# Kernel tuning notes

Measured on AMD Instinct MI355X. Metric: run time of the kernel, lower is better.

Reference implementation:

```python
import jax, jax.numpy as jnp
import numpy as np

NUM_HEADS = 12

def setup_inputs() -> dict:
    key = jax.random.key(0)
    ks = jax.random.split(key, 8)
    B, N, C = 8, 1024, 768
    s = 1.0 / np.sqrt(C)
    return {
        "x": jax.random.normal(ks[0], (B, N, C), jnp.float32),
        "head_mask": jnp.ones((B, NUM_HEADS), jnp.float32),
        "q_w": jax.random.normal(ks[1], (C, C), jnp.float32) * s,
        "q_b": jnp.zeros((C,), jnp.float32),
        "k_w": jax.random.normal(ks[2], (C, C), jnp.float32) * s,
        "k_b": jnp.zeros((C,), jnp.float32),
        "v_w": jax.random.normal(ks[3], (C, C), jnp.float32) * s,
        "v_b": jnp.zeros((C,), jnp.float32),
        "proj_w": jax.random.normal(ks[4], (C, C), jnp.float32) * s,
        "proj_b": jnp.zeros((C,), jnp.float32),
    }

def reference(x, head_mask, q_w, q_b, k_w, k_b, v_w, v_b, proj_w, proj_b):
    B, N, C = x.shape
    H = NUM_HEADS
    d = C // H
    scale = d ** -0.5
    # torch Linear: y = x @ W.T + b; reshape to [B,H,N,d]
    q = (x @ q_w.T + q_b).reshape(B, N, H, d).transpose(0, 2, 1, 3)
    k = (x @ k_w.T + k_b).reshape(B, N, H, d).transpose(0, 2, 1, 3)
    v = (x @ v_w.T + v_b).reshape(B, N, H, d).transpose(0, 2, 1, 3)
    attn = jnp.einsum('bhnd,bhmd->bhnm', q, k) * scale
    attn = jax.nn.softmax(attn, axis=-1)
    y = jnp.einsum('bhnm,bhmd->bhnd', attn, v)
    # head_mask applied per head [B,H,1,1]
    y = y * head_mask[:, :, None, None]
    out = y.transpose(0, 2, 1, 3).reshape(B, N, C)
    # head_mask repeated per head_dim, applied to flattened channels [B,1,C]
    hm_flat = jnp.repeat(head_mask, d, axis=1)[:, None, :]
    out = out * hm_flat
    return out @ proj_w.T + proj_b
```

## Files before the change

### kernel.cpp

```cpp
#include <hip/hip_runtime.h>

typedef _Float16 half_t;
typedef _Float16 half2_t __attribute__((ext_vector_type(2)));
typedef _Float16 half4_t __attribute__((ext_vector_type(4)));
typedef _Float16 half8 __attribute__((ext_vector_type(8)));
typedef float f32x4 __attribute__((ext_vector_type(4)));
typedef float f32x16 __attribute__((ext_vector_type(16)));
typedef unsigned uint4v __attribute__((ext_vector_type(4)));

__device__ __forceinline__ void gload_lds16(const void* g, void* l) {
    __builtin_amdgcn_global_load_lds(
        (const __attribute__((address_space(1))) void*)g,
        (__attribute__((address_space(3))) void*)l, 16, 0, 0);
}

__global__ __launch_bounds__(256) void cast_f32_f16(const float* __restrict__ s,
                                                    half_t* __restrict__ d, int n) {
    const int stride = gridDim.x * blockDim.x;
    for (int i = blockIdx.x * blockDim.x + threadIdx.x; i * 4 < n; i += stride) {
        const float4 v = *(const float4*)(s + (long)i * 4);
        half4_t h = {(half_t)v.x, (half_t)v.y, (half_t)v.z, (half_t)v.w};
        *(half4_t*)(d + (long)i * 4) = h;
    }
}

__global__ __launch_bounds__(256) void cast_w4(const float* __restrict__ w0,
                                               const float* __restrict__ w1,
                                               const float* __restrict__ w2,
                                               const float* __restrict__ w3,
                                               half_t* __restrict__ d) {
    const int i = blockIdx.x * blockDim.x + threadIdx.x;
    const int which = i / 147456;
    const int off = i - which * 147456;
    const float* s = which == 0 ? w0 : which == 1 ? w1 : which == 2 ? w2 : w3;
    const float4 v = *(const float4*)(s + (long)off * 4);
    half4_t h = {(half_t)v.x, (half_t)v.y, (half_t)v.z, (half_t)v.w};
    *(half4_t*)(d + (long)i * 4) = h;
}

__global__ __launch_bounds__(256) void concat_bias(const float* __restrict__ a,
                                                   const float* __restrict__ b,
                                                   const float* __restrict__ c,
                                                   float* __restrict__ o) {
    int i = blockIdx.x * blockDim.x + threadIdx.x;
    if (i < 768) o[i] = a[i];
    else if (i < 1536) o[i] = b[i - 768];
    else if (i < 2304) o[i] = c[i - 1536];
}

template <typename OutT, bool VSPLIT>
__global__ __launch_bounds__(256) void gemm128(const half_t* __restrict__ A,
                                               const half_t* __restrict__ W,
                                               const float* __restrict__ bias,
                                               OutT* __restrict__ C,
                                               half_t* __restrict__ Vt,
                                               const int N) {
    constexpr int Kdim = 768, NT = 12;
    alignas(16) __shared__ half_t Ah[2][128 * 64];
    alignas(16) __shared__ half_t Wh[2][128 * 64];

    const int t = threadIdx.x, l = t & 63, wv = t >> 6;
    const int wr = wv >> 1, wc = wv & 1;
    const int m0 = blockIdx.x * 128, n0 = blockIdx.y * 128;

    f32x4 acc[4][4] = {};

    const int srow_g = wv * 8 + (l >> 3);
    const int schunk = l & 7;

    const half_t* Ag = A + (long)m0 * Kdim;
    const half_t* Wg = W + (long)n0 * Kdim;

    auto STAGE = [&](int tile, int buf) {
        const int k0 = tile * 64;
#pragma unroll
        for (int g = 0; g < 4; ++g) {
            const int row = g * 32 + srow_g;
            const int sc_ = (schunk ^ (row & 7)) * 8;
            gload_lds16(Ag + (long)row * Kdim + k0 + sc_,
                        &Ah[buf][(g * 32 + wv * 8) * 64]);
            gload_lds16(Wg + (long)row * Kdim + k0 + sc_,
                        &Wh[buf][(g * 32 + wv * 8) * 64]);
        }
    };

    STAGE(0, 0);
    STAGE(1, 1);

    for (int tt = 0; tt < NT; ++tt) {
        const int buf = tt & 1;
        if (tt < NT - 1) {
            asm volatile("s_waitcnt vmcnt(8)" ::: "memory");
        } else {
            asm volatile("s_waitcnt vmcnt(0)" ::: "memory");
        }
        __builtin_amdgcn_s_barrier();
        asm volatile("" ::: "memory");

#pragma unroll
        for (int ks = 0; ks < 2; ++ks) {
            const int kc = ks * 4 + (l >> 4);
            half8 afr[4], bfr[4];
#pragma unroll
            for (int i = 0; i < 4; ++i) {
                const int arow = wr * 64 + i * 16 + (l & 15);
                afr[i] = *(const half8*)&Ah[buf][arow * 64 + (kc ^ (arow & 7)) * 8];
                const int brow = wc * 64 + i * 16 + (l & 15);
                bfr[i] = *(const half8*)&Wh[buf][brow * 64 + (kc ^ (brow & 7)) * 8];
            }
            __builtin_amdgcn_s_setprio(1);
#pragma unroll
            for (int mi = 0; mi < 4; ++mi)
#pragma unroll
                for (int ni = 0; ni < 4; ++ni)
                    acc[mi][ni] = __builtin_amdgcn_mfma_f32_16x16x32_f16(
                        afr[mi], bfr[ni], acc[mi][ni], 0, 0, 0);
            __builtin_amdgcn_s_setprio(0);
        }

        asm volatile("" ::: "memory");
        __builtin_amdgcn_s_barrier();
        if (tt + 2 < NT) STAGE(tt + 2, buf);
    }

    const bool vtile = VSPLIT && (blockIdx.y >= 12);
#pragma unroll
    for (int ni = 0; ni < 4; ++ni) {
        const int col = n0 + wc * 64 + ni * 16 + (l & 15);
        const float bb = bias[col];
        if (!vtile) {
#pragma unroll
            for (int mi = 0; mi < 4; ++mi) {
                const int row = m0 + wr * 64 + mi * 16 + (l >> 4) * 4;
#pragma unroll
                for (int r = 0; r < 4; ++r)
                    C[(long)(row + r) * N + col] = (OutT)(acc[mi][ni][r] + bb);
            }
        } else {
            const int hd = col - 1536;
            const int hidx = hd >> 6, d = hd & 63;
#pragma unroll
            for (int mi = 0; mi < 4; ++mi) {
                const int row = m0 + wr * 64 + mi * 16 + (l >> 4) * 4;
                const int b = row >> 10, n = row & 1023;
                half4_t pk;
#pragma unroll
                for (int r = 0; r < 4; ++r) pk[r] = (half_t)(acc[mi][ni][r] + bb);
                *(half4_t*)(Vt + ((long)((b * 12 + hidx) * 64 + d)) * 1024 + n) = pk;
            }
        }
    }
}

__global__ __launch_bounds__(256) void attn5_kernel(const half_t* __restrict__ qkv,
                                                    const half_t* __restrict__ Vt,
                                                    const float* __restrict__ head_mask,
                                                    half_t* __restrict__ Y) {
    alignas(16) __shared__ half_t Kl[2][64 * 64];
    alignas(16) __shared__ half_t Vl[2][64 * 64];

    const int t = threadIdx.x, l = t & 63, wv = t >> 6;
    const int h2 = l >> 5, q32 = l & 31;
    const int bh = blockIdx.x, b = bh / 12, hh = bh % 12;
    const int q0 = blockIdx.y * 128 + wv * 32;

    half8 qf[4];
    {
        const half_t SC = (half_t)(0.125f * 1.44269504f);
        const half_t* Qp = qkv + ((long)(b * 1024 + q0 + q32)) * 2304 + hh * 64 + h2 * 8;
#pragma unroll
        for (int kd = 0; kd < 4; ++kd) {
            half8 v = *(const half8*)(Qp + kd * 16);
#pragma unroll
            for (int j = 0; j < 8; ++j) v[j] = v[j] * SC;
            qf[kd] = v;
        }
    }

    const half8 ONES = {(half_t)1, (half_t)1, (half_t)1, (half_t)1,
                        (half_t)1, (half_t)1, (half_t)1, (half_t)1};

    const half_t* Kg = qkv + (long)b * 1024 * 2304 + 768 + hh * 64;
    const half_t* Vg = Vt + (long)bh * 64 * 1024;

    const int srow_lo = (l >> 3);
    const int schunk = l & 7;

    auto STAGE = [&](int tile, int bf) {
#pragma unroll
        for (int c = 0; c < 2; ++c) {
            const int row = c * 32 + wv * 8 + srow_lo;
            const int sc_ = (schunk ^ (row & 7)) * 8;
            gload_lds16(Kg + (long)(tile * 64 + row) * 2304 + sc_,
                        &Kl[bf][(c * 32 + wv * 8) * 64]);
            gload_lds16(Vg + (long)row * 1024 + tile * 64 + sc_,
                        &Vl[bf][(c * 32 + wv * 8) * 64]);
        }
    };

    f32x16 o0 = {}, o1 = {}, lacc = {};

    STAGE(0, 0);

    for (int tt = 0; tt < 16; ++tt) {
        const int bf = tt & 1;
        if (tt < 15) {
            STAGE(tt + 1, bf ^ 1);
            asm volatile("s_waitcnt vmcnt(4)" ::: "memory");
        } else {
            asm volatile("s_waitcnt vmcnt(0)" ::: "memory");
        }
        __builtin_amdgcn_s_barrier();
        asm volatile("" ::: "memory");

        f32x16 s0 = {}, s1 = {};
        __builtin_amdgcn_s_setprio(1);
#pragma unroll
        for (int kd = 0; kd < 4; ++kd) {
            const int ch = ((kd * 2 + h2) ^ (q32 & 7)) * 8;
            half8 k0 = *(const half8*)&Kl[bf][q32 * 64 + ch];
            half8 k1 = *(const half8*)&Kl[bf][(32 + q32) * 64 + ch];
            s0 = __builtin_amdgcn_mfma_f32_32x32x16_f16(k0, qf[kd], s0, 0, 0, 0);
            s1 = __builtin_amdgcn_mfma_f32_32x32x16_f16(k1, qf[kd], s1, 0, 0, 0);
        }
        __builtin_amdgcn_s_setprio(0);

#pragma unroll
        for (int kc = 0; kc < 4; ++kc) {
            const f32x16& ss = (kc >> 1) ? s1 : s0;
            const int rb = (kc & 1) * 8;
            unsigned pw[4];
#pragma unroll
            for (int k2 = 0; k2 < 4; ++k2) {
                const float a = __builtin_amdgcn_exp2f(ss[rb + 2 * k2]);
                const float c = __builtin_amdgcn_exp2f(ss[rb + 2 * k2 + 1]);
                pw[k2] = __builtin_bit_cast(unsigned, __builtin_amdgcn_cvt_pkrtz(a, c));
            }
            uint4v uu = {pw[0], pw[1], pw[2], pw[3]};
            const half8 pf = __builtin_bit_cast(half8, uu);

            const int g0 = 2 * kc;
            const int a0 = q32 * 64 + ((g0 ^ (q32 & 7)) * 8) + 4 * h2;
            const int a1 = q32 * 64 + (((g0 + 1) ^ (q32 & 7)) * 8) + 4 * h2;
            const int r2 = 32 + q32;
            const int b0 = r2 * 64 + ((g0 ^ (r2 & 7)) * 8) + 4 * h2;
            const int b1 = r2 * 64 + (((g0 + 1) ^ (r2 & 7)) * 8) + 4 * h2;
            half4_t va0 = *(const half4_t*)&Vl[bf][a0];
            half4_t va1 = *(const half4_t*)&Vl[bf][a1];
            half4_t vb0 = *(const half4_t*)&Vl[bf][b0];
            half4_t vb1 = *(const half4_t*)&Vl[bf][b1];
            half8 vf0 = {va0[0], va0[1], va0[2], va0[3], va1[0], va1[1], va1[2], va1[3]};
            half8 vf1 = {vb0[0], vb0[1], vb0[2], vb0[3], vb1[0], vb1[1], vb1[2], vb1[3]};

            __builtin_amdgcn_s_setprio(1);
            o0 = __builtin_amdgcn_mfma_f32_32x32x16_f16(vf0, pf, o0, 0, 0, 0);
            o1 = __builtin_amdgcn_mfma_f32_32x32x16_f16(vf1, pf, o1, 0, 0, 0);
            lacc = __builtin_amdgcn_mfma_f32_32x32x16_f16(ONES, pf, lacc, 0, 0, 0);
            __builtin_amdgcn_s_setprio(0);
        }

        asm volatile("" ::: "memory");
        __builtin_amdgcn_s_barrier();
    }

    const float hmv = head_mask[b * 12 + hh];
    const float sc = hmv * hmv / lacc[0];
    half_t* Yp = Y + ((long)(b * 1024 + q0 + q32)) * 768 + hh * 64;
#pragma unroll
    for (int db = 0; db < 2; ++db) {
        const f32x16 oo = db ? o1 : o0;
#pragma unroll
        for (int rq = 0; rq < 4; ++rq) {
            half4_t pk;
#pragma unroll
            for (int i = 0; i < 4; ++i) pk[i] = (half_t)(oo[rq * 4 + i] * sc);
            *(half4_t*)(Yp + db * 32 + rq * 8 + h2 * 4) = pk;
        }
    }
}

extern "C" void kernel_launch(void* const* d_in, const int* in_sizes, int n_in,
                              void* d_out, int out_size, void* d_ws, size_t ws_size,
                              hipStream_t stream) {
    const float* x   = (const float*)d_in[0];
    const float* hm  = (const float*)d_in[1];
    const float* q_w = (const float*)d_in[2];
    const float* q_b = (const float*)d_in[3];
    const float* k_w = (const float*)d_in[4];
    const float* k_b = (const float*)d_in[5];
    const float* v_w = (const float*)d_in[6];
    const float* v_b = (const float*)d_in[7];
    const float* p_w = (const float*)d_in[8];
    const float* p_b = (const float*)d_in[9];
    float* out = (float*)d_out;

    char* ws = (char*)d_ws;
    half_t* xh  = (half_t*)(ws);
    half_t* wc  = (half_t*)(ws + 12582912);
    half_t* pwh = (half_t*)(ws + 16121856);
    float*  bc  = (float*)(ws + 17301504);
    half_t* qkv = (half_t*)(ws + 17310720);
    half_t* y   = (half_t*)(ws + 55059456);
    half_t* Vt = (ws_size >= (size_t)67642368 + 12582912)
                     ? (half_t*)(ws + 67642368)
                     : (half_t*)d_out;

    cast_f32_f16<<<2048, 256, 0, stream>>>(x, xh, 8192 * 768);
    cast_w4<<<2304, 256, 0, stream>>>(q_w, k_w, v_w, p_w, wc);
    concat_bias<<<9, 256, 0, stream>>>(q_b, k_b, v_b, bc);

    gemm128<half_t, true><<<dim3(64, 18), 256, 0, stream>>>(xh, wc, bc, qkv, Vt, 2304);
    attn5_kernel<<<dim3(96, 8), 256, 0, stream>>>(qkv, Vt, hm, y);
    gemm128<float, false><<<dim3(64, 6), 256, 0, stream>>>(y, pwh, p_b, out, nullptr, 768);
}
```

Before: 114.7 us.

## Permute V token order at GEMM store and merge cast kernels into one launch

```diff
diff --git a/kernel.cpp b/kernel.cpp
--- a/kernel.cpp
+++ b/kernel.cpp
@@ -14,38 +14,36 @@
         (__attribute__((address_space(3))) void*)l, 16, 0, 0);
 }
 
-__global__ __launch_bounds__(256) void cast_f32_f16(const float* __restrict__ s,
-                                                    half_t* __restrict__ d, int n) {
+__global__ __launch_bounds__(256) void megacast(const float* __restrict__ x,
+                                                const float* __restrict__ w0,
+                                                const float* __restrict__ w1,
+                                                const float* __restrict__ w2,
+                                                const float* __restrict__ w3,
+                                                const float* __restrict__ b0,
+                                                const float* __restrict__ b1,
+                                                const float* __restrict__ b2,
+                                                half_t* __restrict__ xh,
+                                                half_t* __restrict__ wc,
+                                                float* __restrict__ bc) {
+    const int tid = blockIdx.x * blockDim.x + threadIdx.x;
+    if (tid < 2304) bc[tid] = tid < 768 ? b0[tid] : tid < 1536 ? b1[tid - 768] : b2[tid - 1536];
     const int stride = gridDim.x * blockDim.x;
-    for (int i = blockIdx.x * blockDim.x + threadIdx.x; i * 4 < n; i += stride) {
-        const float4 v = *(const float4*)(s + (long)i * 4);
+    for (long i = tid; i < 2162688; i += stride) {
+        const float* s;
+        half_t* d;
+        long off;
+        if (i < 1572864) { s = x; d = xh; off = i; }
+        else {
+            const long j = i - 1572864;
+            const int which = (int)(j / 147456);
+            off = j - (long)which * 147456;
+            s = which == 0 ? w0 : which == 1 ? w1 : which == 2 ? w2 : w3;
+            d = wc + (long)which * 589824;
+        }
+        const float4 v = *(const float4*)(s + off * 4);
         half4_t h = {(half_t)v.x, (half_t)v.y, (half_t)v.z, (half_t)v.w};
-        *(half4_t*)(d + (long)i * 4) = h;
-    }
-}
-
-__global__ __launch_bounds__(256) void cast_w4(const float* __restrict__ w0,
-                                               const float* __restrict__ w1,
-                                               const float* __restrict__ w2,
-                                               const float* __restrict__ w3,
-                                               half_t* __restrict__ d) {
-    const int i = blockIdx.x * blockDim.x + threadIdx.x;
-    const int which = i / 147456;
-    const int off = i - which * 147456;
-    const float* s = which == 0 ? w0 : which == 1 ? w1 : which == 2 ? w2 : w3;
-    const float4 v = *(const float4*)(s + (long)off * 4);
-    half4_t h = {(half_t)v.x, (half_t)v.y, (half_t)v.z, (half_t)v.w};
-    *(half4_t*)(d + (long)i * 4) = h;
-}
-
-__global__ __launch_bounds__(256) void concat_bias(const float* __restrict__ a,
-                                                   const float* __restrict__ b,
-                                                   const float* __restrict__ c,
-                                                   float* __restrict__ o) {
-    int i = blockIdx.x * blockDim.x + threadIdx.x;
-    if (i < 768) o[i] = a[i];
-    else if (i < 1536) o[i] = b[i - 768];
-    else if (i < 2304) o[i] = c[i - 1536];
+        *(half4_t*)(d + off * 4) = h;
+    }
 }
 
 template <typename OutT, bool VSPLIT>
@@ -143,16 +141,17 @@
             for (int mi = 0; mi < 4; ++mi) {
                 const int row = m0 + wr * 64 + mi * 16 + (l >> 4) * 4;
                 const int b = row >> 10, n = row & 1023;
+                const int np = (n & ~12) | ((n & 4) << 1) | ((n & 8) >> 1);
                 half4_t pk;
 #pragma unroll
                 for (int r = 0; r < 4; ++r) pk[r] = (half_t)(acc[mi][ni][r] + bb);
-                *(half4_t*)(Vt + ((long)((b * 12 + hidx) * 64 + d)) * 1024 + n) = pk;
+                *(half4_t*)(Vt + ((long)((b * 12 + hidx) * 64 + d)) * 1024 + np) = pk;
             }
         }
     }
 }
 
-__global__ __launch_bounds__(256) void attn5_kernel(const half_t* __restrict__ qkv,
+__global__ __launch_bounds__(256) void attn6_kernel(const half_t* __restrict__ qkv,
                                                     const half_t* __restrict__ Vt,
                                                     const float* __restrict__ head_mask,
                                                     half_t* __restrict__ Y) {
@@ -239,18 +238,9 @@
             uint4v uu = {pw[0], pw[1], pw[2], pw[3]};
             const half8 pf = __builtin_bit_cast(half8, uu);
 
-            const int g0 = 2 * kc;
-            const int a0 = q32 * 64 + ((g0 ^ (q32 & 7)) * 8) + 4 * h2;
-            const int a1 = q32 * 64 + (((g0 + 1) ^ (q32 & 7)) * 8) + 4 * h2;
-            const int r2 = 32 + q32;
-            const int b0 = r2 * 64 + ((g0 ^ (r2 & 7)) * 8) + 4 * h2;
-            const int b1 = r2 * 64 + (((g0 + 1) ^ (r2 & 7)) * 8) + 4 * h2;
-            half4_t va0 = *(const half4_t*)&Vl[bf][a0];
-            half4_t va1 = *(const half4_t*)&Vl[bf][a1];
-            half4_t vb0 = *(const half4_t*)&Vl[bf][b0];
-            half4_t vb1 = *(const half4_t*)&Vl[bf][b1];
-            half8 vf0 = {va0[0], va0[1], va0[2], va0[3], va1[0], va1[1], va1[2], va1[3]};
-            half8 vf1 = {vb0[0], vb0[1], vb0[2], vb0[3], vb1[0], vb1[1], vb1[2], vb1[3]};
+            const int ch = ((2 * kc + h2) ^ (q32 & 7)) * 8;
+            half8 vf0 = *(const half8*)&Vl[bf][q32 * 64 + ch];
+            half8 vf1 = *(const half8*)&Vl[bf][(32 + q32) * 64 + ch];
 
             __builtin_amdgcn_s_setprio(1);
             o0 = __builtin_amdgcn_mfma_f32_32x32x16_f16(vf0, pf, o0, 0, 0, 0);
@@ -305,11 +295,9 @@
                      ? (half_t*)(ws + 67642368)
                      : (half_t*)d_out;
 
-    cast_f32_f16<<<2048, 256, 0, stream>>>(x, xh, 8192 * 768);
-    cast_w4<<<2304, 256, 0, stream>>>(q_w, k_w, v_w, p_w, wc);
-    concat_bias<<<9, 256, 0, stream>>>(q_b, k_b, v_b, bc);
+    megacast<<<2048, 256, 0, stream>>>(x, q_w, k_w, v_w, p_w, q_b, k_b, v_b, xh, wc, bc);
 
     gemm128<half_t, true><<<dim3(64, 18), 256, 0, stream>>>(xh, wc, bc, qkv, Vt, 2304);
-    attn5_kernel<<<dim3(96, 8), 256, 0, stream>>>(qkv, Vt, hm, y);
+    attn6_kernel<<<dim3(96, 8), 256, 0, stream>>>(qkv, Vt, hm, y);
     gemm128<float, false><<<dim3(64, 6), 256, 0, stream>>>(y, pwh, p_b, out, nullptr, 768);
 }
```

New measurement: 109.2 us. 4.8% less time.
